# Kernel tuning notes

Hardware: AMD Instinct MI355X
Metric: run time of the kernel (lower is better)

The kernel has to match this reference:

```python
import jax, jax.numpy as jnp
import numpy as np

N_NODES = 100000
N_EDGES = 1600000
NFEAT, NHID, NCLASS = 128, 64, 16


def setup_inputs() -> dict:
    key = jax.random.key(0)
    ks = jax.random.split(key, 8)
    x = jax.random.normal(ks[0], (N_NODES, NFEAT), dtype=jnp.float32)
    src = jax.random.randint(ks[1], (N_EDGES,), 0, N_NODES, dtype=jnp.int32)
    dst = jax.random.randint(ks[2], (N_EDGES,), 0, N_NODES, dtype=jnp.int32)
    edge_weight = jax.random.uniform(ks[3], (N_EDGES,), dtype=jnp.float32)
    W1 = jax.random.normal(ks[4], (NFEAT, NHID), dtype=jnp.float32) / np.sqrt(NFEAT)
    b1 = jnp.zeros((NHID,), dtype=jnp.float32)
    W2 = jax.random.normal(ks[5], (NHID, NCLASS), dtype=jnp.float32) / np.sqrt(NHID)
    b2 = jnp.zeros((NCLASS,), dtype=jnp.float32)
    return {"x": x, "src": src, "dst": dst, "edge_weight": edge_weight,
            "W1": W1, "b1": b1, "W2": W2, "b2": b2}


def _spmm(src, dst, edge_weight, support):
    # out[i] = sum_{e: dst[e]==i} w[e] * support[src[e]]   (adj @ support)
    msgs = edge_weight[:, None] * support[src]  # [E, d]
    return jax.ops.segment_sum(msgs, dst, num_segments=N_NODES)


def reference(x, src, dst, edge_weight, W1, b1, W2, b2):
    # layer 1: dense projection then sparse aggregation, relu
    h = jax.nn.relu(_spmm(src, dst, edge_weight, x @ W1) + b1)  # [N, nhid]
    # layer 2: identity activation
    logits = _spmm(src, dst, edge_weight, h @ W2) + b2          # [N, nclass]
    return jax.nn.log_softmax(logits, axis=1)
```

## Files before the change

### kernel.cpp

```cpp
#include <hip/hip_runtime.h>

#define N_NODES 100000
#define N_EDGES 1600000
#define NFEAT 128
#define NHID 64
#define NCLASS 16

#define BSHIFT 7
#define BUCK_NODES 128
#define NBUCK ((N_NODES + BUCK_NODES - 1) >> BSHIFT)
#define ECAP 2560
#define EDGE_TILE 8192
#define NB_SCAT ((N_EDGES + EDGE_TILE - 1) / EDGE_TILE)
#define EPT 16
#define NB_GEMM ((N_NODES + 127) / 128)

#define HPAD 66

#define SCALE1 262144.0f
#define INV_SCALE1 (1.0f / 262144.0f)
#define SCALE2 131072.0f
#define INV_SCALE2 (1.0f / 131072.0f)

#define BIASF 4194304.0f
#define BIASSH 22

typedef __attribute__((ext_vector_type(8))) short short8;
typedef __attribute__((ext_vector_type(4))) float float4v;
typedef unsigned long long u64t;

__device__ __forceinline__ float bflo(unsigned int u) {
    return __uint_as_float(u << 16);
}
__device__ __forceinline__ float bfhi(unsigned int u) {
    return __uint_as_float(u & 0xFFFF0000u);
}
__device__ __forceinline__ unsigned short f2bf(float f) {
    unsigned int b = __float_as_uint(f);
    b += 0x7FFFu + ((b >> 16) & 1u);
    return (unsigned short)(b >> 16);
}
__device__ __forceinline__ unsigned int fxb(float ws, float bf) {
    return (unsigned int)__float2int_rn(fmaf(ws, bf, BIASF));
}
__device__ __forceinline__ void pk2(u64t* hp, unsigned int lo, unsigned int hi) {
    atomicAdd(hp, ((u64t)hi << 32) | (u64t)lo);
}
__device__ __forceinline__ void pkadd8(int* hrow_f0, uint4 u, float ws) {
    u64t* hp = (u64t*)hrow_f0;
    pk2(hp + 0, fxb(ws, bflo(u.x)), fxb(ws, bfhi(u.x)));
    pk2(hp + 1, fxb(ws, bflo(u.y)), fxb(ws, bfhi(u.y)));
    pk2(hp + 2, fxb(ws, bflo(u.z)), fxb(ws, bfhi(u.z)));
    pk2(hp + 3, fxb(ws, bflo(u.w)), fxb(ws, bfhi(u.w)));
}

__global__ __launch_bounds__(512) void k_gemm1_scatter(
        const float* __restrict__ x, const float* __restrict__ W1,
        unsigned short* __restrict__ s1,
        const int* __restrict__ dst, const int* __restrict__ src,
        const float* __restrict__ ew,
        int* __restrict__ fill, int2* __restrict__ edgeA) {
    __shared__ unsigned short w1t[64][136];
    __shared__ int hist[NBUCK], bbase[NBUCK], bfill[NBUCK];

    if (blockIdx.x >= NB_GEMM) {
        for (int i = threadIdx.x; i < NBUCK; i += 512) { hist[i] = 0; bfill[i] = 0; }

        const int bid  = blockIdx.x - NB_GEMM;
        const int base = bid * EDGE_TILE;
        int   d[EPT]; int s[EPT]; float w[EPT]; bool v[EPT];
#pragma unroll
        for (int k = 0; k < EPT; ++k) {
            int e = base + threadIdx.x + k * 512;
            v[k] = e < N_EDGES;
            d[k] = v[k] ? dst[e] : 0;
        }
#pragma unroll
        for (int k = 0; k < EPT; ++k) {
            int e = base + threadIdx.x + k * 512;
            s[k] = v[k] ? src[e] : 0;
        }
#pragma unroll
        for (int k = 0; k < EPT; ++k) {
            int e = base + threadIdx.x + k * 512;
            w[k] = v[k] ? ew[e] : 0.f;
        }
        __syncthreads();

#pragma unroll
        for (int k = 0; k < EPT; ++k)
            if (v[k]) atomicAdd(&hist[d[k] >> BSHIFT], 1);
        __syncthreads();

        {
            int rot = (bid * 53) % NBUCK;
            for (int i = threadIdx.x; i < NBUCK; i += 512) {
                int j = i + rot;
                if (j >= NBUCK) j -= NBUCK;
                bbase[j] = hist[j] ? atomicAdd(&fill[j], hist[j]) : 0;
            }
        }
        __syncthreads();

#pragma unroll
        for (int k = 0; k < EPT; ++k) {
            if (v[k]) {
                int bb = d[k] >> BSHIFT;
                int r  = bbase[bb] + atomicAdd(&bfill[bb], 1);
                if (r < ECAP)
                    edgeA[(size_t)bb * ECAP + r] =
                        make_int2(s[k] | ((d[k] & (BUCK_NODES - 1)) << 17),
                                  __float_as_int(w[k]));
            }
        }
        return;
    }

    for (int i = threadIdx.x; i < NFEAT * NHID; i += 512) {
        int n = i & 63, k = i >> 6;
        w1t[n][k] = f2bf(W1[k * NHID + n]);
    }
    __syncthreads();

    const int lane = threadIdx.x & 63;
    const int wv   = threadIdx.x >> 6;
    const int m    = lane & 15;
    const int quad = lane >> 4;
    const int node0 = blockIdx.x * 128 + wv * 16;
    if (node0 >= N_NODES) return;

    short8 bfrag[4][4];
#pragma unroll
    for (int kt = 0; kt < 4; ++kt)
#pragma unroll
        for (int nt = 0; nt < 4; ++nt)
            bfrag[kt][nt] = *(const short8*)&w1t[nt * 16 + m][kt * 32 + quad * 8];

    const float4* xr = (const float4*)(x + (size_t)node0 * NFEAT);
    float4v acc[4] = {{0.f,0.f,0.f,0.f},{0.f,0.f,0.f,0.f},
                      {0.f,0.f,0.f,0.f},{0.f,0.f,0.f,0.f}};
#pragma unroll
    for (int kt = 0; kt < 4; ++kt) {
        float4 f0 = xr[m * 32 + kt * 8 + quad * 2];
        float4 f1 = xr[m * 32 + kt * 8 + quad * 2 + 1];
        short8 a;
        a[0] = (short)f2bf(f0.x); a[1] = (short)f2bf(f0.y);
        a[2] = (short)f2bf(f0.z); a[3] = (short)f2bf(f0.w);
        a[4] = (short)f2bf(f1.x); a[5] = (short)f2bf(f1.y);
        a[6] = (short)f2bf(f1.z); a[7] = (short)f2bf(f1.w);
#pragma unroll
        for (int nt = 0; nt < 4; ++nt)
            acc[nt] = __builtin_amdgcn_mfma_f32_16x16x32_bf16(
                a, bfrag[kt][nt], acc[nt], 0, 0, 0);
    }
#pragma unroll
    for (int nt = 0; nt < 4; ++nt)
#pragma unroll
        for (int i = 0; i < 4; ++i)
            s1[(size_t)(node0 + quad * 4 + i) * NHID + nt * 16 + m] =
                f2bf(acc[nt][i]);
}

__global__ __launch_bounds__(512) void k_bagg1(const int* __restrict__ cnt,
                                               const int2* __restrict__ edgeA,
                                               const unsigned short* __restrict__ s1,
                                               const float* __restrict__ b1,
                                               const float* __restrict__ W2,
                                               unsigned short* __restrict__ s2) {
    __shared__ int h[BUCK_NODES][HPAD];
    const int b = blockIdx.x;
    for (int i = threadIdx.x; i < BUCK_NODES * HPAD; i += 512)
        ((int*)h)[i] = 0;
    __syncthreads();

    const int beg = b * ECAP;
    int c = cnt[b]; if (c > ECAP) c = ECAP;
    const int end = beg + c;
    const uint4* __restrict__ s1u4 = (const uint4*)s1;
    const int sg = threadIdx.x >> 3;
    const int r  = threadIdx.x & 7;
    const int f0 = r * 8;

    int p = beg + sg;
    for (; p + 448 < end; p += 512) {
        int2 e[8];
#pragma unroll
        for (int k = 0; k < 8; ++k) e[k] = edgeA[p + 64 * k];
        uint4 u[8];
#pragma unroll
        for (int k = 0; k < 8; ++k)
            u[k] = s1u4[(size_t)(e[k].x & 0x1FFFF) * 8 + r];
#pragma unroll
        for (int k = 0; k < 8; ++k) {
            float ws = __int_as_float(e[k].y) * SCALE1;
            int  ld = e[k].x >> 17;
            pkadd8(&h[ld][f0], u[k], ws);
            if (r == 0) atomicAdd(&h[ld][64], 1);
        }
    }
    for (; p + 192 < end; p += 256) {
        int2 e[4];
#pragma unroll
        for (int k = 0; k < 4; ++k) e[k] = edgeA[p + 64 * k];
        uint4 u[4];
#pragma unroll
        for (int k = 0; k < 4; ++k)
            u[k] = s1u4[(size_t)(e[k].x & 0x1FFFF) * 8 + r];
#pragma unroll
        for (int k = 0; k < 4; ++k) {
            float ws = __int_as_float(e[k].y) * SCALE1;
            int  ld = e[k].x >> 17;
            pkadd8(&h[ld][f0], u[k], ws);
            if (r == 0) atomicAdd(&h[ld][64], 1);
        }
    }
    for (; p < end; p += 64) {
        int2 e = edgeA[p];
        uint4 u = s1u4[(size_t)(e.x & 0x1FFFF) * 8 + r];
        float ws = __int_as_float(e.y) * SCALE1;
        int ld = e.x >> 17;
        pkadd8(&h[ld][f0], u, ws);
        if (r == 0) atomicAdd(&h[ld][64], 1);
    }
    __syncthreads();

    const int wv   = threadIdx.x >> 6;
    const int lane = threadIdx.x & 63;
    const int m    = lane & 15;
    const int quad = lane >> 4;
    const int node0 = b << BSHIFT;

    short8 bfr[2];
    float  b1v[2][8];
#pragma unroll
    for (int kt = 0; kt < 2; ++kt)
#pragma unroll
        for (int j = 0; j < 8; ++j) {
            int k = kt * 32 + quad * 8 + j;
            bfr[kt][j] = (short)f2bf(W2[k * NCLASS + m]);
            b1v[kt][j] = b1[k];
        }
    {
        const int row = wv * 16 + m;
        const unsigned int db = ((unsigned int)h[row][64]) << BIASSH;
        float4v acc = {0.f, 0.f, 0.f, 0.f};
#pragma unroll
        for (int kt = 0; kt < 2; ++kt) {
            short8 a;
#pragma unroll
            for (int j = 0; j < 8; ++j) {
                int val = (int)((unsigned int)h[row][kt * 32 + quad * 8 + j] - db);
                a[j] = (short)f2bf(fmaxf((float)val * INV_SCALE1 + b1v[kt][j], 0.f));
            }
            acc = __builtin_amdgcn_mfma_f32_16x16x32_bf16(a, bfr[kt], acc, 0, 0, 0);
        }
        const int nr = node0 + wv * 16 + quad * 4;
#pragma unroll
        for (int i = 0; i < 4; ++i)
            if (nr + i < N_NODES)
                s2[(size_t)(nr + i) * NCLASS + m] = f2bf(acc[i]);
    }
}

__global__ __launch_bounds__(512) void k_bagg2(const int* __restrict__ cnt,
                                               const int2* __restrict__ edgeA,
                                               const unsigned short* __restrict__ s2,
                                               const float* __restrict__ b2,
                                               float* __restrict__ out) {
    __shared__ int h2[BUCK_NODES][18];
    const int b = blockIdx.x;
    for (int i = threadIdx.x; i < BUCK_NODES * 18; i += 512)
        ((int*)h2)[i] = 0;
    __syncthreads();

    const int beg = b * ECAP;
    int c = cnt[b]; if (c > ECAP) c = ECAP;
    const int end = beg + c;
    const unsigned int* __restrict__ s2u = (const unsigned int*)s2;
    const int sg = threadIdx.x >> 3;
    const int r  = threadIdx.x & 7;

    int p = beg + sg;
    for (; p + 448 < end; p += 512) {
        int2 e[8];
#pragma unroll
        for (int k = 0; k < 8; ++k) e[k] = edgeA[p + 64 * k];
        unsigned int u[8];
#pragma unroll
        for (int k = 0; k < 8; ++k)
            u[k] = s2u[(size_t)(e[k].x & 0x1FFFF) * 8 + r];
#pragma unroll
        for (int k = 0; k < 8; ++k) {
            float ws = __int_as_float(e[k].y) * SCALE2;
            int  ld = e[k].x >> 17;
            pk2((u64t*)&h2[ld][0] + r, fxb(ws, bflo(u[k])), fxb(ws, bfhi(u[k])));
            if (r == 0) atomicAdd(&h2[ld][16], 1);
        }
    }
    for (; p + 192 < end; p += 256) {
        int2 e[4];
#pragma unroll
        for (int k = 0; k < 4; ++k) e[k] = edgeA[p + 64 * k];
        unsigned int u[4];
#pragma unroll
        for (int k = 0; k < 4; ++k)
            u[k] = s2u[(size_t)(e[k].x & 0x1FFFF) * 8 + r];
#pragma unroll
        for (int k = 0; k < 4; ++k) {
            float ws = __int_as_float(e[k].y) * SCALE2;
            int  ld = e[k].x >> 17;
            pk2((u64t*)&h2[ld][0] + r, fxb(ws, bflo(u[k])), fxb(ws, bfhi(u[k])));
            if (r == 0) atomicAdd(&h2[ld][16], 1);
        }
    }
    for (; p < end; p += 64) {
        int2 e = edgeA[p];
        unsigned int u = s2u[(size_t)(e.x & 0x1FFFF) * 8 + r];
        float ws = __int_as_float(e.y) * SCALE2;
        int ld = e.x >> 17;
        pk2((u64t*)&h2[ld][0] + r, fxb(ws, bflo(u)), fxb(ws, bfhi(u)));
        if (r == 0) atomicAdd(&h2[ld][16], 1);
    }
    __syncthreads();

    if (threadIdx.x < BUCK_NODES) {
        const int n = (b << BSHIFT) + threadIdx.x;
        if (n < N_NODES) {
            const unsigned int db = ((unsigned int)h2[threadIdx.x][16]) << BIASSH;
            float v[NCLASS];
            float mx = -1e30f;
#pragma unroll
            for (int cc = 0; cc < NCLASS; ++cc) {
                int val = (int)((unsigned int)h2[threadIdx.x][cc] - db);
                v[cc] = (float)val * INV_SCALE2 + b2[cc];
                mx = fmaxf(mx, v[cc]);
            }
            float s = 0.f;
#pragma unroll
            for (int cc = 0; cc < NCLASS; ++cc) s += __expf(v[cc] - mx);
            float ls = mx + __logf(s);
            float* o = out + (size_t)n * NCLASS;
#pragma unroll
            for (int cc = 0; cc < NCLASS; cc += 4) {
                float4 o4 = make_float4(v[cc] - ls, v[cc + 1] - ls,
                                        v[cc + 2] - ls, v[cc + 3] - ls);
                *(float4*)(o + cc) = o4;
            }
        }
    }
}

extern "C" void kernel_launch(void* const* d_in, const int* in_sizes, int n_in,
                              void* d_out, int out_size, void* d_ws, size_t ws_size,
                              hipStream_t stream) {
    const float* x   = (const float*)d_in[0];
    const int*   src = (const int*)d_in[1];
    const int*   dst = (const int*)d_in[2];
    const float* ew  = (const float*)d_in[3];
    const float* W1  = (const float*)d_in[4];
    const float* b1  = (const float*)d_in[5];
    const float* W2  = (const float*)d_in[6];
    const float* b2  = (const float*)d_in[7];
    float* out = (float*)d_out;

    unsigned short* s1 = (unsigned short*)d_ws;
    unsigned short* s2 = s1 + (size_t)N_NODES * NHID;
    int2* edgeA        = (int2*)(s2 + (size_t)N_NODES * NCLASS);
    int*  fill         = (int*)(edgeA + (size_t)NBUCK * ECAP);

    hipMemsetAsync(fill, 0, sizeof(int) * NBUCK, stream);

    k_gemm1_scatter<<<NB_GEMM + NB_SCAT, 512, 0, stream>>>(x, W1, s1, dst, src, ew,
                                                           fill, edgeA);
    k_bagg1<<<NBUCK, 512, 0, stream>>>(fill, edgeA, s1, b1, W2, s2);
    k_bagg2<<<NBUCK, 512, 0, stream>>>(fill, edgeA, s2, b2, out);
}
```

Before: 181.5 us.

## Pad bucket fill counters, double scatter tile, run scatter blocks first, defer src/weight loads

Each bucket's global fill counter now sits on its own 64-byte slot, so global atomics from different blocks no longer contend on shared cache lines. The edge tile per scatter block doubles (32 edges per thread), halving the number of scatter blocks and global atomic reservations. Scatter blocks are now placed ahead of the GEMM blocks in the grid, and the src and weight loads move after the histogram phase in chunks of 8 to hold down register pressure. The cost is fewer, longer scatter blocks, which may lower parallelism and occupancy, plus a larger fill buffer to clear.

```diff
diff --git a/kernel.cpp b/kernel.cpp
--- a/kernel.cpp
+++ b/kernel.cpp
@@ -10,10 +10,11 @@
 #define BUCK_NODES 128
 #define NBUCK ((N_NODES + BUCK_NODES - 1) >> BSHIFT)
 #define ECAP 2560
-#define EDGE_TILE 8192
+#define EDGE_TILE 16384
 #define NB_SCAT ((N_EDGES + EDGE_TILE - 1) / EDGE_TILE)
-#define EPT 16
+#define EPT 32
 #define NB_GEMM ((N_NODES + 127) / 128)
+#define FSTRIDE 16
 
 #define HPAD 66
 
@@ -63,28 +64,18 @@
     __shared__ unsigned short w1t[64][136];
     __shared__ int hist[NBUCK], bbase[NBUCK], bfill[NBUCK];
 
-    if (blockIdx.x >= NB_GEMM) {
+    if (blockIdx.x < NB_SCAT) {
         for (int i = threadIdx.x; i < NBUCK; i += 512) { hist[i] = 0; bfill[i] = 0; }
 
-        const int bid  = blockIdx.x - NB_GEMM;
+        const int bid  = blockIdx.x;
         const int base = bid * EDGE_TILE;
-        int   d[EPT]; int s[EPT]; float w[EPT]; bool v[EPT];
+        int d[EPT]; bool v[EPT];
 #pragma unroll
         for (int k = 0; k < EPT; ++k) {
             int e = base + threadIdx.x + k * 512;
             v[k] = e < N_EDGES;
             d[k] = v[k] ? dst[e] : 0;
         }
-#pragma unroll
-        for (int k = 0; k < EPT; ++k) {
-            int e = base + threadIdx.x + k * 512;
-            s[k] = v[k] ? src[e] : 0;
-        }
-#pragma unroll
-        for (int k = 0; k < EPT; ++k) {
-            int e = base + threadIdx.x + k * 512;
-            w[k] = v[k] ? ew[e] : 0.f;
-        }
         __syncthreads();
 
 #pragma unroll
@@ -93,29 +84,40 @@
         __syncthreads();
 
         {
-            int rot = (bid * 53) % NBUCK;
+            int rot = (bid * 8) % NBUCK;
             for (int i = threadIdx.x; i < NBUCK; i += 512) {
                 int j = i + rot;
                 if (j >= NBUCK) j -= NBUCK;
-                bbase[j] = hist[j] ? atomicAdd(&fill[j], hist[j]) : 0;
+                bbase[j] = hist[j] ? atomicAdd(&fill[j * FSTRIDE], hist[j]) : 0;
             }
         }
         __syncthreads();
 
 #pragma unroll
-        for (int k = 0; k < EPT; ++k) {
-            if (v[k]) {
-                int bb = d[k] >> BSHIFT;
-                int r  = bbase[bb] + atomicAdd(&bfill[bb], 1);
-                if (r < ECAP)
-                    edgeA[(size_t)bb * ECAP + r] =
-                        make_int2(s[k] | ((d[k] & (BUCK_NODES - 1)) << 17),
-                                  __float_as_int(w[k]));
+        for (int c = 0; c < EPT; c += 8) {
+            int   s8[8]; float w8[8];
+#pragma unroll
+            for (int k = 0; k < 8; ++k) {
+                int e = base + threadIdx.x + (c + k) * 512;
+                s8[k] = v[c + k] ? src[e] : 0;
+                w8[k] = v[c + k] ? ew[e]  : 0.f;
+            }
+#pragma unroll
+            for (int k = 0; k < 8; ++k) {
+                if (v[c + k]) {
+                    int bb = d[c + k] >> BSHIFT;
+                    int r  = bbase[bb] + atomicAdd(&bfill[bb], 1);
+                    if (r < ECAP)
+                        edgeA[(size_t)bb * ECAP + r] =
+                            make_int2(s8[k] | ((d[c + k] & (BUCK_NODES - 1)) << 17),
+                                      __float_as_int(w8[k]));
+                }
             }
         }
         return;
     }
 
+    const int gb = blockIdx.x - NB_SCAT;
     for (int i = threadIdx.x; i < NFEAT * NHID; i += 512) {
         int n = i & 63, k = i >> 6;
         w1t[n][k] = f2bf(W1[k * NHID + n]);
@@ -126,7 +128,7 @@
     const int wv   = threadIdx.x >> 6;
     const int m    = lane & 15;
     const int quad = lane >> 4;
-    const int node0 = blockIdx.x * 128 + wv * 16;
+    const int node0 = gb * 128 + wv * 16;
     if (node0 >= N_NODES) return;
 
     short8 bfrag[4][4];
@@ -174,7 +176,7 @@
     __syncthreads();
 
     const int beg = b * ECAP;
-    int c = cnt[b]; if (c > ECAP) c = ECAP;
+    int c = cnt[b * FSTRIDE]; if (c > ECAP) c = ECAP;
     const int end = beg + c;
     const uint4* __restrict__ s1u4 = (const uint4*)s1;
     const int sg = threadIdx.x >> 3;
@@ -274,7 +276,7 @@
     __syncthreads();
 
     const int beg = b * ECAP;
-    int c = cnt[b]; if (c > ECAP) c = ECAP;
+    int c = cnt[b * FSTRIDE]; if (c > ECAP) c = ECAP;
     const int end = beg + c;
     const unsigned int* __restrict__ s2u = (const unsigned int*)s2;
     const int sg = threadIdx.x >> 3;
@@ -368,7 +370,7 @@
     int2* edgeA        = (int2*)(s2 + (size_t)N_NODES * NCLASS);
     int*  fill         = (int*)(edgeA + (size_t)NBUCK * ECAP);
 
-    hipMemsetAsync(fill, 0, sizeof(int) * NBUCK, stream);
+    hipMemsetAsync(fill, 0, sizeof(int) * NBUCK * FSTRIDE, stream);
 
     k_gemm1_scatter<<<NB_GEMM + NB_SCAT, 512, 0, stream>>>(x, W1, s1, dst, src, ew,
                                                            fill, edgeA);
```

New measurement: 188.6 us. 1.04x slower.
